# Optimization experiments

Measured on AMD Instinct MI355X. Metric: run time of the kernel, lower is better.

The kernel has to match this reference:

```python
import jax, jax.numpy as jnp
import numpy as np

B, T, D, K = 8, 4096, 256, 8192

def setup_inputs() -> dict:
    key = jax.random.key(0)
    k1, k2 = jax.random.split(key)
    z = jax.random.normal(k1, (B, T, D), dtype=jnp.float32)
    codebook = jax.random.normal(k2, (K, D), dtype=jnp.float32)
    return {"z": z, "codebook": codebook}

def reference(z, codebook):
    Bm, Tm, Dm = z.shape
    z_flat = z.reshape(-1, Dm)                      # [N, D]
    z_norm_sq = jnp.sum(z_flat * z_flat, axis=1, keepdims=True)   # [N, 1]
    c_norm_sq = jnp.sum(codebook * codebook, axis=1)              # [K]
    dot = jnp.einsum('nd,kd->nk', z_flat, codebook)               # [N, K]
    distances = z_norm_sq + c_norm_sq - 2.0 * dot                 # [N, K]
    indices = jnp.argmin(distances, axis=-1)                      # [N]
    q_flat = codebook[indices]                                    # [N, D] gather
    q_z = q_flat.reshape(Bm, Tm, Dm)
    return q_z, indices.reshape(Bm, Tm)
```

## Files before the change

### kernel.cpp

```cpp
#include <hip/hip_runtime.h>
#include <hip/hip_bf16.h>

#define N_ROWS 32768
#define DDIM   256
#define KCODES 8192
#define QZ     (N_ROWS * DDIM)
#define NTILES 128
#define MARGIN 0.8f

typedef __attribute__((ext_vector_type(8))) short short8;
typedef __attribute__((ext_vector_type(4))) float f32x4;

__device__ __forceinline__ unsigned short f2bf(float f) {
  unsigned u = __builtin_bit_cast(unsigned, f);
  u += 0x7FFFu + ((u >> 16) & 1u);
  return (unsigned short)(u >> 16);
}

__device__ __forceinline__ void ins(float& b1, float& b2, float& b3, int& i1, int& i2,
                                    float d, int c) {
  bool l3 = d < b3, l2 = d < b2, l1 = d < b1;
  b3 = l3 ? (l2 ? b2 : d) : b3;
  b2 = l2 ? (l1 ? b1 : d) : b2;
  i2 = l2 ? (l1 ? i1 : c) : i2;
  b1 = l1 ? d : b1;
  i1 = l1 ? c : i1;
}

__device__ __forceinline__ void merge3(float& a1, float& a2, float& a3, int& x1, int& x2,
                                       float o1, float o2, float o3, int y1, int y2) {
  bool oW = o1 < a1;
  float mx1 = oW ? a1 : o1;  int mxi = oW ? x1 : y1;
  float n1  = oW ? o1 : a1;  int ni1 = oW ? y1 : x1;
  bool lA = a2 < o2;
  float lo2 = lA ? a2 : o2;  int li2 = lA ? x2 : y2;
  float hi2 = lA ? o2 : a2;
  bool m2w = mx1 < lo2;
  float n2 = m2w ? mx1 : lo2; int ni2 = m2w ? mxi : li2;
  float n3 = fminf(fminf(fmaxf(mx1, lo2), hi2), fminf(a3, o3));
  a1 = n1; a2 = n2; a3 = n3; x1 = ni1; x2 = ni2;
}

__global__ __launch_bounds__(256) void vq_cnorm(const float* __restrict__ cb,
                                                float* __restrict__ cn) {
  int n = blockIdx.x * 4 + (threadIdx.x >> 6);
  int lane = threadIdx.x & 63;
  float4 c4 = *reinterpret_cast<const float4*>(cb + (size_t)n * DDIM + lane * 4);
  double s = (double)c4.x * c4.x + (double)c4.y * c4.y +
             (double)c4.z * c4.z + (double)c4.w * c4.w;
  #pragma unroll
  for (int off = 32; off > 0; off >>= 1) s += __shfl_down(s, off, 64);
  if (lane == 0) cn[n] = (float)s;
}

__global__ __launch_bounds__(256) void vq_prep(const float* __restrict__ cb,
                                               unsigned char* __restrict__ wcb,
                                               float* __restrict__ cn) {
  int n = blockIdx.x * 4 + (threadIdx.x >> 6);
  int lane = threadIdx.x & 63;
  float4 c4 = *reinterpret_cast<const float4*>(cb + (size_t)n * DDIM + lane * 4);
  double s = (double)c4.x * c4.x + (double)c4.y * c4.y +
             (double)c4.z * c4.z + (double)c4.w * c4.w;
  #pragma unroll
  for (int off = 32; off > 0; off >>= 1) s += __shfl_down(s, off, 64);
  if (lane == 0) cn[n] = (float)s;

  unsigned short h0 = f2bf(c4.x), h1 = f2bf(c4.y), h2 = f2bf(c4.z), h3 = f2bf(c4.w);
  size_t base = (size_t)n * 512 +
                (size_t)((((lane >> 1) ^ (n & 7)) << 4) + (lane & 1) * 8);
  *reinterpret_cast<ushort4*>(wcb + base) = make_ushort4(h0, h1, h2, h3);
}

__global__ __launch_bounds__(256, 2) void vq_mfma(
    const float* __restrict__ z, const unsigned char* __restrict__ wcb,
    const float* __restrict__ cn, const float* __restrict__ cb,
    float* __restrict__ out,
    int* __restrict__ cntA, int4* __restrict__ rowsA,
    int* __restrict__ cntB, int* __restrict__ rowsB) {
  __shared__ __align__(16) unsigned char cs[2][32768];
  __shared__ float rb1[2][64], rb2[2][64], rb3[2][64];
  __shared__ int   ri1[2][64], ri2[2][64];
  __shared__ int   sIdx[64];

  const int tid = threadIdx.x;
  const int w = tid >> 6, lane = tid & 63;
  const int wm = w >> 1, wn = w & 1;
  const int g = lane >> 4, l15 = lane & 15;

  short8 zh[2][8];
  const int rA = blockIdx.x * 64 + wm * 32 + l15;
  #pragma unroll
  for (int mf = 0; mf < 2; ++mf) {
    #pragma unroll
    for (int dc = 0; dc < 8; ++dc) {
      const float* zp = z + (size_t)(rA + mf * 16) * DDIM + dc * 32 + g * 8;
      float4 f0 = *reinterpret_cast<const float4*>(zp);
      float4 f1 = *reinterpret_cast<const float4*>(zp + 4);
      short8 hh;
      hh[0] = (short)f2bf(f0.x); hh[1] = (short)f2bf(f0.y);
      hh[2] = (short)f2bf(f0.z); hh[3] = (short)f2bf(f0.w);
      hh[4] = (short)f2bf(f1.x); hh[5] = (short)f2bf(f1.y);
      hh[6] = (short)f2bf(f1.z); hh[7] = (short)f2bf(f1.w);
      zh[mf][dc] = hh;
    }
  }

  float b1[8], b2[8], b3[8];
  int i1[8], i2[8];
  #pragma unroll
  for (int s = 0; s < 8; ++s) { b1[s] = 3.4e38f; b2[s] = 3.4e38f; b3[s] = 3.4e38f; i1[s] = 0; i2[s] = 0; }

  #pragma unroll
  for (int i = 0; i < 8; ++i) {
    __builtin_amdgcn_global_load_lds(
        (const __attribute__((address_space(1))) void*)(wcb + tid * 16 + i * 4096),
        (__attribute__((address_space(3))) void*)(&cs[0][tid * 16 + i * 4096]), 16, 0, 0);
  }
  __syncthreads();

  const int cc0 = wn * 32 + l15;
  const int cc1 = cc0 + 16;
  const int swz = cc0 & 7;

  for (int nt = 0; nt < NTILES; ++nt) {
    const int cur = nt & 1;
    if (nt + 1 < NTILES) {
      const unsigned char* gsrc = wcb + (size_t)(nt + 1) * 32768;
      #pragma unroll
      for (int i = 0; i < 8; ++i) {
        __builtin_amdgcn_global_load_lds(
            (const __attribute__((address_space(1))) void*)(gsrc + tid * 16 + i * 4096),
            (__attribute__((address_space(3))) void*)(&cs[cur ^ 1][tid * 16 + i * 4096]), 16, 0, 0);
      }
    }

    int code0 = nt * 64 + cc0;
    float cn0 = cn[code0];
    float cn1 = cn[code0 + 16];

    const unsigned char* lb = cs[cur];
    f32x4 a00 = {0.f, 0.f, 0.f, 0.f}, a01 = a00, a10 = a00, a11 = a00;
    #pragma unroll
    for (int dc = 0; dc < 8; ++dc) {
      int u = dc * 4 + g;
      int o0 = cc0 * 512 + ((u ^ swz) << 4);
      int o1 = cc1 * 512 + ((u ^ swz) << 4);
      short8 c0 = *reinterpret_cast<const short8*>(lb + o0);
      short8 c1 = *reinterpret_cast<const short8*>(lb + o1);
      a00 = __builtin_amdgcn_mfma_f32_16x16x32_bf16(zh[0][dc], c0, a00, 0, 0, 0);
      a01 = __builtin_amdgcn_mfma_f32_16x16x32_bf16(zh[0][dc], c1, a01, 0, 0, 0);
      a10 = __builtin_amdgcn_mfma_f32_16x16x32_bf16(zh[1][dc], c0, a10, 0, 0, 0);
      a11 = __builtin_amdgcn_mfma_f32_16x16x32_bf16(zh[1][dc], c1, a11, 0, 0, 0);
    }

    #pragma unroll
    for (int mf = 0; mf < 2; ++mf) {
      const f32x4 an0 = mf ? a10 : a00;
      const f32x4 an1 = mf ? a11 : a01;
      #pragma unroll
      for (int r = 0; r < 4; ++r) {
        const int s = mf * 4 + r;
        float d0 = fmaf(-2.0f, an0[r], cn0);
        ins(b1[s], b2[s], b3[s], i1[s], i2[s], d0, code0);
        float d1 = fmaf(-2.0f, an1[r], cn1);
        ins(b1[s], b2[s], b3[s], i1[s], i2[s], d1, code0 + 16);
      }
    }
    __syncthreads();
  }

  #pragma unroll
  for (int s = 0; s < 8; ++s) {
    float B1 = b1[s], B2 = b2[s], B3 = b3[s];
    int I1 = i1[s], I2 = i2[s];
    #pragma unroll
    for (int m = 1; m <= 8; m <<= 1) {
      float o1 = __shfl_xor(B1, m, 64), o2 = __shfl_xor(B2, m, 64), o3 = __shfl_xor(B3, m, 64);
      int y1 = __shfl_xor(I1, m, 64), y2 = __shfl_xor(I2, m, 64);
      merge3(B1, B2, B3, I1, I2, o1, o2, o3, y1, y2);
    }
    if (l15 == 0) {
      int row = wm * 32 + (s >> 2) * 16 + g * 4 + (s & 3);
      rb1[wn][row] = B1; rb2[wn][row] = B2; rb3[wn][row] = B3;
      ri1[wn][row] = I1; ri2[wn][row] = I2;
    }
  }
  __syncthreads();

  if (tid < 64) {
    float B1 = rb1[0][tid], B2 = rb2[0][tid], B3 = rb3[0][tid];
    int I1 = ri1[0][tid], I2 = ri2[0][tid];
    merge3(B1, B2, B3, I1, I2, rb1[1][tid], rb2[1][tid], rb3[1][tid], ri1[1][tid], ri2[1][tid]);
    int grow = blockIdx.x * 64 + tid;
    out[QZ + grow] = (float)I1;
    sIdx[tid] = I1;
    if (B3 - B1 < MARGIN) {
      int p = atomicAdd(cntB, 1);
      rowsB[p] = grow;
    } else if (B2 - B1 < MARGIN) {
      int p = atomicAdd(cntA, 1);
      rowsA[p] = make_int4(grow, I1, I2, 0);
    }
  }
  __syncthreads();

  #pragma unroll
  for (int i = 0; i < 16; ++i) {
    int f = tid + i * 256;
    int r = f >> 6, c4i = f & 63;
    float4 v = *reinterpret_cast<const float4*>(cb + (size_t)sIdx[r] * DDIM + c4i * 4);
    *reinterpret_cast<float4*>(&out[(size_t)(blockIdx.x * 64 + r) * DDIM + c4i * 4]) = v;
  }
}

__global__ __launch_bounds__(256) void vq_pairs(
    const float* __restrict__ z, const float* __restrict__ cb, const float* __restrict__ cn,
    float* __restrict__ out, const int* __restrict__ cntA, const int4* __restrict__ rowsA) {
  int n = *cntA;
  int lane = threadIdx.x & 63;
  for (int e = blockIdx.x * 4 + (threadIdx.x >> 6); e < n; e += gridDim.x * 4) {
    int4 ent = rowsA[e];
    int row = ent.x, c1 = ent.y, c2 = ent.z;
    float4 zv = *reinterpret_cast<const float4*>(z + (size_t)row * DDIM + lane * 4);
    float4 a = *reinterpret_cast<const float4*>(cb + (size_t)c1 * DDIM + lane * 4);
    float4 b = *reinterpret_cast<const float4*>(cb + (size_t)c2 * DDIM + lane * 4);
    float p1 = zv.x * a.x + zv.y * a.y + zv.z * a.z + zv.w * a.w;
    float p2 = zv.x * b.x + zv.y * b.y + zv.z * b.z + zv.w * b.w;
    #pragma unroll
    for (int m = 1; m <= 32; m <<= 1) { p1 += __shfl_xor(p1, m, 64); p2 += __shfl_xor(p2, m, 64); }
    float d1 = cn[c1] - 2.0f * p1;
    float d2 = cn[c2] - 2.0f * p2;
    int win = (d2 < d1 || (d2 == d1 && c2 < c1)) ? c2 : c1;
    if (lane == 0) out[QZ + row] = (float)win;
    float4 cw = *reinterpret_cast<const float4*>(cb + (size_t)win * DDIM + lane * 4);
    *reinterpret_cast<float4*>(&out[(size_t)row * DDIM + lane * 4]) = cw;
  }
}

#define FS_CODES 128
#define FS_PAD   257
__global__ __launch_bounds__(256) void vq_fullsweep(
    const float* __restrict__ z, const float* __restrict__ cb, const float* __restrict__ cn,
    const int* __restrict__ cntB, const int* __restrict__ rowsB,
    unsigned long long* __restrict__ keysB) {
  __shared__ float csL[FS_CODES * FS_PAD];
  __shared__ float zr[DDIM];
  __shared__ float part[4][FS_CODES];
  const int nB = *cntB;
  if (nB == 0) return;
  const int cid = blockIdx.x & 63;
  const int sid = blockIdx.x >> 6;
  const int t = threadIdx.x;
  const int q = t >> 6, k = t & 63;

  const float* src = cb + (size_t)cid * FS_CODES * DDIM;
  #pragma unroll
  for (int i = 0; i < 32; ++i) {
    int f = t + i * 256;
    int code = f >> 6, j = f & 63;
    float4 v = *reinterpret_cast<const float4*>(src + (size_t)f * 4);
    *reinterpret_cast<float4*>(&csL[code * FS_PAD + j * 4]) = v;
  }
  float cnk = (t < FS_CODES) ? cn[cid * FS_CODES + t] : 0.f;

  for (int r = sid; r < nB; r += 4) {
    const int row = rowsB[r];
    __syncthreads();
    if (t < 64)
      *reinterpret_cast<float4*>(&zr[t * 4]) =
          *reinterpret_cast<const float4*>(z + (size_t)row * DDIM + t * 4);
    __syncthreads();

    float acc0 = 0.f, acc1 = 0.f;
    #pragma unroll
    for (int j = 0; j < 16; ++j) {
      float4 a  = *reinterpret_cast<const float4*>(&zr[q * 64 + j * 4]);
      float4 c0 = *reinterpret_cast<const float4*>(&csL[k * FS_PAD + q * 64 + j * 4]);
      float4 c1 = *reinterpret_cast<const float4*>(&csL[(k + 64) * FS_PAD + q * 64 + j * 4]);
      acc0 = fmaf(a.x, c0.x, acc0); acc0 = fmaf(a.y, c0.y, acc0);
      acc0 = fmaf(a.z, c0.z, acc0); acc0 = fmaf(a.w, c0.w, acc0);
      acc1 = fmaf(a.x, c1.x, acc1); acc1 = fmaf(a.y, c1.y, acc1);
      acc1 = fmaf(a.z, c1.z, acc1); acc1 = fmaf(a.w, c1.w, acc1);
    }
    part[q][k] = acc0;
    part[q][k + 64] = acc1;
    __syncthreads();

    if (t < FS_CODES) {
      float dot = part[0][t] + part[1][t] + part[2][t] + part[3][t];
      float d = cnk - 2.0f * dot;
      int code = cid * FS_CODES + t;
      unsigned m = __builtin_bit_cast(unsigned, d);
      m = (m >> 31) ? ~m : (m | 0x80000000u);
      unsigned long long key = ((unsigned long long)m << 32) | (unsigned)code;
      #pragma unroll
      for (int mm = 1; mm <= 32; mm <<= 1) {
        unsigned long long o = __shfl_xor(key, mm, 64);
        key = (o < key) ? o : key;
      }
      if (k == 0) atomicMin(&keysB[r], key);
    }
  }
}

__global__ __launch_bounds__(256) void vq_finishB(
    const float* __restrict__ cb, float* __restrict__ out,
    const int* __restrict__ cntB, const int* __restrict__ rowsB,
    const unsigned long long* __restrict__ keysB) {
  int nB = *cntB;
  int lane = threadIdx.x & 63;
  for (int e = blockIdx.x * 4 + (threadIdx.x >> 6); e < nB; e += gridDim.x * 4) {
    int row = rowsB[e];
    int idx = (int)(keysB[e] & 0xFFFFFFFFULL);
    if (lane == 0) out[QZ + row] = (float)idx;
    *reinterpret_cast<float4*>(&out[(size_t)row * DDIM + lane * 4]) =
        *reinterpret_cast<const float4*>(cb + (size_t)idx * DDIM + lane * 4);
  }
}

#define FB_BM 64
#define FB_BK 32
#define FB_LD 260
__global__ __launch_bounds__(256) void vq_main_fb(const float* __restrict__ z,
                                                  const float* __restrict__ cb,
                                                  const float* __restrict__ cn,
                                                  float* __restrict__ out) {
  __shared__ float zs[FB_BM * FB_LD];
  __shared__ float csh[FB_BK * FB_LD];
  __shared__ float redd[FB_BM][16];
  __shared__ int   redi[FB_BM][16];
  __shared__ int   sidx[FB_BM];
  const int t = threadIdx.x;
  const int row0 = blockIdx.x * FB_BM;
  #pragma unroll
  for (int i = 0; i < 16; ++i) {
    int f = t + i * 256; int r = f >> 6, c4 = f & 63;
    *reinterpret_cast<float4*>(&zs[r * FB_LD + c4 * 4]) =
        *reinterpret_cast<const float4*>(z + (size_t)(row0 + r) * DDIM + c4 * 4);
  }
  const int tr = t >> 4, tc = t & 15;
  float best[4]; int bidx[4];
  #pragma unroll
  for (int i = 0; i < 4; ++i) { best[i] = 3.4e38f; bidx[i] = 0; }
  for (int kt = 0; kt < KCODES; kt += FB_BK) {
    __syncthreads();
    #pragma unroll
    for (int i = 0; i < 8; ++i) {
      int f = t + i * 256; int r = f >> 6, c4 = f & 63;
      *reinterpret_cast<float4*>(&csh[r * FB_LD + c4 * 4]) =
          *reinterpret_cast<const float4*>(cb + (size_t)(kt + r) * DDIM + c4 * 4);
    }
    __syncthreads();
    float acc[4][2] = {{0.f,0.f},{0.f,0.f},{0.f,0.f},{0.f,0.f}};
    #pragma unroll 8
    for (int d4 = 0; d4 < 64; ++d4) {
      float4 b0 = *reinterpret_cast<const float4*>(&csh[tc * FB_LD + d4 * 4]);
      float4 b1v = *reinterpret_cast<const float4*>(&csh[(tc + 16) * FB_LD + d4 * 4]);
      #pragma unroll
      for (int i = 0; i < 4; ++i) {
        float4 a = *reinterpret_cast<const float4*>(&zs[(4 * tr + i) * FB_LD + d4 * 4]);
        acc[i][0] = fmaf(a.x, b0.x, acc[i][0]); acc[i][0] = fmaf(a.y, b0.y, acc[i][0]);
        acc[i][0] = fmaf(a.z, b0.z, acc[i][0]); acc[i][0] = fmaf(a.w, b0.w, acc[i][0]);
        acc[i][1] = fmaf(a.x, b1v.x, acc[i][1]); acc[i][1] = fmaf(a.y, b1v.y, acc[i][1]);
        acc[i][1] = fmaf(a.z, b1v.z, acc[i][1]); acc[i][1] = fmaf(a.w, b1v.w, acc[i][1]);
      }
    }
    float cn0 = cn[kt + tc], cn1 = cn[kt + tc + 16];
    #pragma unroll
    for (int i = 0; i < 4; ++i) {
      float d0 = cn0 - 2.0f * acc[i][0];
      if (d0 < best[i]) { best[i] = d0; bidx[i] = kt + tc; }
      float d1 = cn1 - 2.0f * acc[i][1];
      if (d1 < best[i]) { best[i] = d1; bidx[i] = kt + tc + 16; }
    }
  }
  #pragma unroll
  for (int i = 0; i < 4; ++i) { redd[4 * tr + i][tc] = best[i]; redi[4 * tr + i][tc] = bidx[i]; }
  __syncthreads();
  if (t < FB_BM) {
    float bd = redd[t][0]; int bi = redi[t][0];
    #pragma unroll
    for (int j = 1; j < 16; ++j) {
      float d = redd[t][j]; int ix = redi[t][j];
      if (d < bd || (d == bd && ix < bi)) { bd = d; bi = ix; }
    }
    sidx[t] = bi;
    out[QZ + row0 + t] = (float)bi;
  }
  __syncthreads();
  #pragma unroll
  for (int i = 0; i < 16; ++i) {
    int f = t + i * 256; int r = f >> 6, c4 = f & 63;
    *reinterpret_cast<float4*>(&out[(size_t)(row0 + r) * DDIM + c4 * 4]) =
        *reinterpret_cast<const float4*>(cb + (size_t)sidx[r] * DDIM + c4 * 4);
  }
}

extern "C" void kernel_launch(void* const* d_in, const int* in_sizes, int n_in,
                              void* d_out, int out_size, void* d_ws, size_t ws_size,
                              hipStream_t stream) {
  const float* z  = (const float*)d_in[0];
  const float* cb = (const float*)d_in[1];
  float* out = (float*)d_out;

  const size_t OFF_CN   = (size_t)KCODES * 512;
  const size_t OFF_CNT  = OFF_CN + (size_t)KCODES * 4;
  const size_t OFF_RA   = OFF_CNT + 16;
  const size_t OFF_RB   = OFF_RA + (size_t)N_ROWS * 16;
  const size_t OFF_KEYS = OFF_RB + (size_t)N_ROWS * 4;
  const size_t NEED     = OFF_KEYS + (size_t)N_ROWS * 8;

  if (ws_size >= NEED) {
    unsigned char* wcb = (unsigned char*)d_ws;
    float* cn = (float*)(wcb + OFF_CN);
    int* cntA = (int*)(wcb + OFF_CNT);
    int* cntB = (int*)(wcb + OFF_CNT + 4);
    int4* rowsA = (int4*)(wcb + OFF_RA);
    int* rowsB = (int*)(wcb + OFF_RB);
    unsigned long long* keysB = (unsigned long long*)(wcb + OFF_KEYS);
    hipMemsetAsync(cntA, 0, 8, stream);
    hipMemsetAsync(keysB, 0xFF, (size_t)N_ROWS * 8, stream);
    vq_prep<<<KCODES / 4, 256, 0, stream>>>(cb, wcb, cn);
    vq_mfma<<<N_ROWS / 64, 256, 0, stream>>>(z, wcb, cn, cb, out,
                                             cntA, rowsA, cntB, rowsB);
    vq_pairs<<<128, 256, 0, stream>>>(z, cb, cn, out, cntA, rowsA);
    vq_fullsweep<<<256, 256, 0, stream>>>(z, cb, cn, cntB, rowsB, keysB);
    vq_finishB<<<64, 256, 0, stream>>>(cb, out, cntB, rowsB, keysB);
  } else {
    float* cn = (float*)d_ws;
    vq_cnorm<<<KCODES / 4, 256, 0, stream>>>(cb, cn);
    vq_main_fb<<<N_ROWS / FB_BM, 256, 0, stream>>>(z, cb, cn, out);
  }
}
```

Before: 476.3 us.

## Stream codebook tiles directly from global into registers, dropping LDS staging

The prep kernel now lays out the bf16 codebook in per-16-code fragment order, so each lane reads its MFMA B operand straight from global memory with coalesced 16-byte loads. The main kernel drops the shared-memory double buffer and the per-tile block barriers. Each wave pair now splits the codebook in half, with software-pipelined register prefetch of alternating tiles. This trades LDS traffic and sync for more global/L2 reads, since each wave loads its own B fragments, and for a higher register count.

```diff
diff --git a/kernel.cpp b/kernel.cpp
--- a/kernel.cpp
+++ b/kernel.cpp
@@ -5,7 +5,7 @@
 #define DDIM   256
 #define KCODES 8192
 #define QZ     (N_ROWS * DDIM)
-#define NTILES 128
+#define NT_W   256
 #define MARGIN 0.8f
 
 typedef __attribute__((ext_vector_type(8))) short short8;
@@ -66,8 +66,8 @@
   if (lane == 0) cn[n] = (float)s;
 
   unsigned short h0 = f2bf(c4.x), h1 = f2bf(c4.y), h2 = f2bf(c4.z), h3 = f2bf(c4.w);
-  size_t base = (size_t)n * 512 +
-                (size_t)((((lane >> 1) ^ (n & 7)) << 4) + (lane & 1) * 8);
+  size_t base = (size_t)(n >> 4) * 8192 + (size_t)(lane >> 1) * 256 +
+                (size_t)(n & 15) * 16 + (size_t)(lane & 1) * 8;
   *reinterpret_cast<ushort4*>(wcb + base) = make_ushort4(h0, h1, h2, h3);
 }
 
@@ -77,14 +77,13 @@
     float* __restrict__ out,
     int* __restrict__ cntA, int4* __restrict__ rowsA,
     int* __restrict__ cntB, int* __restrict__ rowsB) {
-  __shared__ __align__(16) unsigned char cs[2][32768];
   __shared__ float rb1[2][64], rb2[2][64], rb3[2][64];
   __shared__ int   ri1[2][64], ri2[2][64];
   __shared__ int   sIdx[64];
 
   const int tid = threadIdx.x;
   const int w = tid >> 6, lane = tid & 63;
-  const int wm = w >> 1, wn = w & 1;
+  const int wm = w >> 1, wh = w & 1;
   const int g = lane >> 4, l15 = lane & 15;
 
   short8 zh[2][8];
@@ -110,64 +109,44 @@
   #pragma unroll
   for (int s = 0; s < 8; ++s) { b1[s] = 3.4e38f; b2[s] = 3.4e38f; b3[s] = 3.4e38f; i1[s] = 0; i2[s] = 0; }
 
-  #pragma unroll
-  for (int i = 0; i < 8; ++i) {
-    __builtin_amdgcn_global_load_lds(
-        (const __attribute__((address_space(1))) void*)(wcb + tid * 16 + i * 4096),
-        (__attribute__((address_space(3))) void*)(&cs[0][tid * 16 + i * 4096]), 16, 0, 0);
-  }
-  __syncthreads();
-
-  const int cc0 = wn * 32 + l15;
-  const int cc1 = cc0 + 16;
-  const int swz = cc0 & 7;
-
-  for (int nt = 0; nt < NTILES; ++nt) {
-    const int cur = nt & 1;
-    if (nt + 1 < NTILES) {
-      const unsigned char* gsrc = wcb + (size_t)(nt + 1) * 32768;
-      #pragma unroll
-      for (int i = 0; i < 8; ++i) {
-        __builtin_amdgcn_global_load_lds(
-            (const __attribute__((address_space(1))) void*)(gsrc + tid * 16 + i * 4096),
-            (__attribute__((address_space(3))) void*)(&cs[cur ^ 1][tid * 16 + i * 4096]), 16, 0, 0);
-      }
-    }
-
-    int code0 = nt * 64 + cc0;
-    float cn0 = cn[code0];
-    float cn1 = cn[code0 + 16];
-
-    const unsigned char* lb = cs[cur];
-    f32x4 a00 = {0.f, 0.f, 0.f, 0.f}, a01 = a00, a10 = a00, a11 = a00;
-    #pragma unroll
-    for (int dc = 0; dc < 8; ++dc) {
-      int u = dc * 4 + g;
-      int o0 = cc0 * 512 + ((u ^ swz) << 4);
-      int o1 = cc1 * 512 + ((u ^ swz) << 4);
-      short8 c0 = *reinterpret_cast<const short8*>(lb + o0);
-      short8 c1 = *reinterpret_cast<const short8*>(lb + o1);
-      a00 = __builtin_amdgcn_mfma_f32_16x16x32_bf16(zh[0][dc], c0, a00, 0, 0, 0);
-      a01 = __builtin_amdgcn_mfma_f32_16x16x32_bf16(zh[0][dc], c1, a01, 0, 0, 0);
-      a10 = __builtin_amdgcn_mfma_f32_16x16x32_bf16(zh[1][dc], c0, a10, 0, 0, 0);
-      a11 = __builtin_amdgcn_mfma_f32_16x16x32_bf16(zh[1][dc], c1, a11, 0, 0, 0);
-    }
-
-    #pragma unroll
-    for (int mf = 0; mf < 2; ++mf) {
-      const f32x4 an0 = mf ? a10 : a00;
-      const f32x4 an1 = mf ? a11 : a01;
-      #pragma unroll
-      for (int r = 0; r < 4; ++r) {
-        const int s = mf * 4 + r;
-        float d0 = fmaf(-2.0f, an0[r], cn0);
-        ins(b1[s], b2[s], b3[s], i1[s], i2[s], d0, code0);
-        float d1 = fmaf(-2.0f, an1[r], cn1);
-        ins(b1[s], b2[s], b3[s], i1[s], i2[s], d1, code0 + 16);
-      }
-    }
-    __syncthreads();
-  }
+  const short8* bp = reinterpret_cast<const short8*>(wcb) +
+                     ((size_t)(wh * 256) * 512) + lane;
+  const int ccbase = wh * 4096 + l15;
+
+#define LOADT(dst, nt_) do {                                         \
+    const short8* tp = bp + ((size_t)(nt_) * 512);                   \
+    _Pragma("unroll")                                                \
+    for (int i_ = 0; i_ < 8; ++i_) dst[i_] = tp[i_ * 64];            \
+  } while (0)
+
+#define COMPT(B_, nt_) do {                                          \
+    const int cc_ = ccbase + (nt_) * 16;                             \
+    const float cnv_ = cn[cc_];                                      \
+    f32x4 a0_ = {0.f, 0.f, 0.f, 0.f}, a1_ = a0_;                     \
+    _Pragma("unroll")                                                \
+    for (int dc_ = 0; dc_ < 8; ++dc_) {                              \
+      a0_ = __builtin_amdgcn_mfma_f32_16x16x32_bf16(zh[0][dc_], B_[dc_], a0_, 0, 0, 0); \
+      a1_ = __builtin_amdgcn_mfma_f32_16x16x32_bf16(zh[1][dc_], B_[dc_], a1_, 0, 0, 0); \
+    }                                                                \
+    _Pragma("unroll")                                                \
+    for (int r_ = 0; r_ < 4; ++r_) {                                 \
+      float d0_ = fmaf(-2.0f, a0_[r_], cnv_);                        \
+      ins(b1[r_], b2[r_], b3[r_], i1[r_], i2[r_], d0_, cc_);         \
+      float d1_ = fmaf(-2.0f, a1_[r_], cnv_);                        \
+      ins(b1[4 + r_], b2[4 + r_], b3[4 + r_], i1[4 + r_], i2[4 + r_], d1_, cc_); \
+    }                                                                \
+  } while (0)
+
+  short8 Ba[8], Bb[8];
+  LOADT(Ba, 0);
+  for (int nt = 0; nt < NT_W; nt += 2) {
+    LOADT(Bb, nt + 1);
+    COMPT(Ba, nt);
+    if (nt + 2 < NT_W) LOADT(Ba, nt + 2);
+    COMPT(Bb, nt + 1);
+  }
+#undef LOADT
+#undef COMPT
 
   #pragma unroll
   for (int s = 0; s < 8; ++s) {
@@ -181,8 +160,8 @@
     }
     if (l15 == 0) {
       int row = wm * 32 + (s >> 2) * 16 + g * 4 + (s & 3);
-      rb1[wn][row] = B1; rb2[wn][row] = B2; rb3[wn][row] = B3;
-      ri1[wn][row] = I1; ri2[wn][row] = I2;
+      rb1[wh][row] = B1; rb2[wh][row] = B2; rb3[wh][row] = B3;
+      ri1[wh][row] = I1; ri2[wh][row] = I2;
     }
   }
   __syncthreads();
```

Measured after the change: 431.5 us. 9.4% less time.
